# Kernel optimization log

Hardware: AMD Instinct MI355X
Metric: run time of the kernel (lower is better)

## Reference

```python
import jax, jax.numpy as jnp
import numpy as np

L, T, D, H, V, TY, FF = 24, 2048, 512, 16, 1025, 512, 2048
DH = D // H
TOP_K = 15
REP_PEN = 1.35


def _layernorm(x, g, b):
    mu = jnp.mean(x, -1, keepdims=True)
    var = jnp.var(x, -1, keepdims=True)
    return (x - mu) / jnp.sqrt(var + 1e-5) * g + b


def _sine_pe(n, d):
    pos = jnp.arange(n, dtype=jnp.float32)[:, None]
    div = jnp.exp(jnp.arange(0, d, 2, dtype=jnp.float32) * (-np.log(10000.0) / d))
    pe = jnp.zeros((n, d), jnp.float32)
    pe = pe.at[:, 0::2].set(jnp.sin(pos * div))
    pe = pe.at[:, 1::2].set(jnp.cos(pos * div))
    return pe


def setup_inputs() -> dict:
    key = jax.random.key(0)
    ks = jax.random.split(key, 12)
    s = 0.02
    return {
        'y': jax.random.randint(ks[0], (1, TY), 0, V - 1),
        'k_cache': jax.random.normal(ks[1], (L, T, D), jnp.float32),
        'v_cache': jax.random.normal(ks[2], (L, T, D), jnp.float32),
        'y_emb': jax.random.normal(ks[3], (1, TY, D), jnp.float32),
        'tok_emb': jax.random.normal(ks[4], (V, D), jnp.float32) * s,
        'alpha': jnp.ones((1,), jnp.float32),
        'qkv_w': jax.random.normal(ks[5], (L, D, 3 * D), jnp.float32) * s,
        'qkv_b': jnp.zeros((L, 3 * D), jnp.float32),
        'out_w': jax.random.normal(ks[6], (L, D, D), jnp.float32) * s,
        'out_b': jnp.zeros((L, D), jnp.float32),
        'ln1_g': jnp.ones((L, D), jnp.float32),
        'ln1_b': jnp.zeros((L, D), jnp.float32),
        'ff1_w': jax.random.normal(ks[7], (L, D, FF), jnp.float32) * s,
        'ff1_b': jnp.zeros((L, FF), jnp.float32),
        'ff2_w': jax.random.normal(ks[8], (L, FF, D), jnp.float32) * s,
        'ff2_b': jnp.zeros((L, D), jnp.float32),
        'ln2_g': jnp.ones((L, D), jnp.float32),
        'ln2_b': jnp.zeros((L, D), jnp.float32),
        'pred_w': jax.random.normal(ks[9], (D, V), jnp.float32) * s,
    }


def reference(y, k_cache, v_cache, y_emb, tok_emb, alpha, qkv_w, qkv_b, out_w, out_b,
              ln1_g, ln1_b, ff1_w, ff1_b, ff2_w, ff2_b, ln2_g, ln2_b, pred_w):
    # --- embed last generated token, extend y_emb, add learned-alpha sine PE ---
    e = tok_emb[y[0, -1]]                                   # [D]
    y_emb_new = jnp.concatenate([y_emb, e[None, None, :]], axis=1)  # [1, TY+1, D]
    pe = _sine_pe(y_emb_new.shape[1], D)
    y_pos = y_emb_new + alpha[0] * pe[None]
    x = y_pos[0, -1]                                        # [D] single query token

    inv = 1.0 / np.sqrt(DH)

    def step(x, per):
        (qw, qb, ow, ob, g1, b1, w1, bb1, w2, bb2, g2, b2, kl, vl) = per
        qkv = x @ qw + qb
        q, kn, vn = qkv[:D], qkv[D:2 * D], qkv[2 * D:]
        k_all = jnp.concatenate([kl, kn[None]], 0).reshape(-1, H, DH)  # [T+1,H,DH]
        v_all = jnp.concatenate([vl, vn[None]], 0).reshape(-1, H, DH)
        att = jax.nn.softmax(jnp.einsum('hd,thd->ht', q.reshape(H, DH), k_all) * inv, axis=-1)
        o = jnp.einsum('ht,thd->hd', att, v_all).reshape(D)
        x = _layernorm(x + o @ ow + ob, g1, b1)             # post-norm (norm_first=False)
        ff = jax.nn.relu(x @ w1 + bb1) @ w2 + bb2
        x = _layernorm(x + ff, g2, b2)
        return x, (kn, vn)

    xs = (qkv_w, qkv_b, out_w, out_b, ln1_g, ln1_b, ff1_w, ff1_b,
          ff2_w, ff2_b, ln2_g, ln2_b, k_cache, v_cache)
    x, (k_new, v_new) = jax.lax.scan(step, x, xs)

    logits = x @ pred_w                                     # [V]

    # --- sampling pipeline: repetition penalty -> (top_p=1.0 skip) -> top_k -> softmax ---
    prev = y[0]
    score = logits[prev]
    score = jnp.where(score < 0, score * REP_PEN, score / REP_PEN)
    logits = logits.at[prev].set(score)
    vals = jax.lax.top_k(logits, TOP_K)[0]
    logits = jnp.where(logits < vals[-1], -jnp.inf, logits)
    probs = jax.nn.softmax(logits)
    # faithful to torch code: divide probs by standard-normal noise and argmax
    noise = jax.random.normal(jax.random.key(42), (V,), jnp.float32)
    idx_next = jnp.argmax(probs / noise).astype(jnp.int32)
    return probs, idx_next, k_new, v_new
```

## Files before the change

kernel.cpp:

```cpp
#include <hip/hip_runtime.h>
#include <math.h>


#define LNUM 24
#define TPOS 2048
#define DMOD 512
#define HNUM 16
#define VOC  1025
#define TYN  512
#define FFD  2048
#define DHD  32
#define NBLK 256
#define NTHR 256

#define INV_SQRT_DH 0.17677669529663687f


__device__ __forceinline__ unsigned rotl32(unsigned x, int d) {
    return (x << d) | (x >> (32 - d));
}

__device__ float threefry_normal(int i) {
    unsigned c0 = 0u;
    unsigned c1 = (unsigned)i;
    unsigned ks[3];
    ks[0] = 0u; ks[1] = 42u; ks[2] = 0x1BD11BDAu ^ ks[0] ^ ks[1];
    unsigned x0 = c0 + ks[0];
    unsigned x1 = c1 + ks[1];
    const int r0[4] = {13, 15, 26, 6};
    const int r1[4] = {17, 29, 16, 24};
    #pragma unroll
    for (int g = 0; g < 5; ++g) {
        const int* rr = (g & 1) ? r1 : r0;
        #pragma unroll
        for (int j = 0; j < 4; ++j) {
            x0 += x1; x1 = rotl32(x1, rr[j]); x1 ^= x0;
        }
        x0 += ks[(g + 1) % 3];
        x1 += ks[(g + 2) % 3] + (unsigned)(g + 1);
    }
    unsigned bits = x0 ^ x1;
    float u01 = __uint_as_float((bits >> 9) | 0x3f800000u) - 1.0f;
    const float lo = -0.99999994f;
    float u = u01 * (1.0f - lo) + lo;
    u = fmaxf(lo, u);
    float w = -log1pf(-u * u);
    float pp;
    if (w < 5.0f) {
        w = w - 2.5f;
        pp = 2.81022636e-08f;
        pp = fmaf(pp, w, 3.43273939e-07f);
        pp = fmaf(pp, w, -3.5233877e-06f);
        pp = fmaf(pp, w, -4.39150654e-06f);
        pp = fmaf(pp, w, 0.00021858087f);
        pp = fmaf(pp, w, -0.00125372503f);
        pp = fmaf(pp, w, -0.00417768164f);
        pp = fmaf(pp, w, 0.246640727f);
        pp = fmaf(pp, w, 1.50140941f);
    } else {
        w = sqrtf(w) - 3.0f;
        pp = -0.000200214257f;
        pp = fmaf(pp, w, 0.000100950558f);
        pp = fmaf(pp, w, 0.00134934322f);
        pp = fmaf(pp, w, -0.00367342844f);
        pp = fmaf(pp, w, 0.00573950773f);
        pp = fmaf(pp, w, -0.0076224613f);
        pp = fmaf(pp, w, 0.00943887047f);
        pp = fmaf(pp, w, 1.00167406f);
        pp = fmaf(pp, w, 2.83297682f);
    }
    return 1.4142135623730951f * pp * u;
}

__global__ void zero_kernel(float* p, int n) {
    int i = blockIdx.x * blockDim.x + threadIdx.x;
    if (i < n) p[i] = 0.0f;
}

__device__ __forceinline__ float wave_red_sum(float v) {
    #pragma unroll
    for (int o = 32; o; o >>= 1) v += __shfl_xor(v, o, 64);
    return v;
}
__device__ __forceinline__ float wave_red_max(float v) {
    #pragma unroll
    for (int o = 32; o; o >>= 1) v = fmaxf(v, __shfl_xor(v, o, 64));
    return v;
}
__device__ __forceinline__ float block_sum(float v, float* red8, int tid) {
    v = wave_red_sum(v);
    __syncthreads();
    if ((tid & 63) == 0) red8[tid >> 6] = v;
    __syncthreads();
    return red8[0] + red8[1] + red8[2] + red8[3];
}
__device__ __forceinline__ float block_max(float v, float* red8, int tid) {
    v = wave_red_max(v);
    __syncthreads();
    if ((tid & 63) == 0) red8[tid >> 6] = v;
    __syncthreads();
    return fmaxf(fmaxf(red8[0], red8[1]), fmaxf(red8[2], red8[3]));
}

__device__ __forceinline__ float gloadf(const float* p) {
    return __hip_atomic_load((float*)p, __ATOMIC_RELAXED, __HIP_MEMORY_SCOPE_AGENT);
}
__device__ __forceinline__ void gstoref(float* p, float v) {
    __hip_atomic_store(p, v, __ATOMIC_RELAXED, __HIP_MEMORY_SCOPE_AGENT);
}

__device__ __forceinline__ void gsync(unsigned* goB, unsigned* arr,
                                      unsigned& epoch, int tid, int blk) {
    __syncthreads();
    ++epoch;
    if (blk == 0) {
        if (tid > 0) {
            while (__hip_atomic_load(&arr[tid * 16], __ATOMIC_RELAXED,
                                     __HIP_MEMORY_SCOPE_AGENT) < epoch)
                __builtin_amdgcn_s_sleep(1);
        }
        __syncthreads();
        if (tid > 0)
            __hip_atomic_store(&goB[tid * 16], epoch, __ATOMIC_RELAXED,
                               __HIP_MEMORY_SCOPE_AGENT);
    } else {
        if (tid == 0) {
            __hip_atomic_store(&arr[blk * 16], epoch, __ATOMIC_RELAXED,
                               __HIP_MEMORY_SCOPE_AGENT);
            while (__hip_atomic_load(&goB[blk * 16], __ATOMIC_RELAXED,
                                     __HIP_MEMORY_SCOPE_AGENT) < epoch)
                __builtin_amdgcn_s_sleep(1);
        }
        __syncthreads();
    }
}

__device__ __forceinline__ void ln_into(const float* __restrict__ u, const float* __restrict__ g,
                                        const float* __restrict__ b, float* xs, float* red8, int tid) {
    float a = gloadf(u + tid), c = gloadf(u + tid + 256);
    float s1 = block_sum(a + c, red8, tid);
    float s2 = block_sum(a * a + c * c, red8, tid);
    float mu = s1 * (1.0f / DMOD);
    float var = s2 * (1.0f / DMOD) - mu * mu;
    float rstd = rsqrtf(var + 1e-5f);
    xs[tid]       = (a - mu) * rstd * g[tid] + b[tid];
    xs[tid + 256] = (c - mu) * rstd * g[tid + 256] + b[tid + 256];
    __syncthreads();
}

__device__ __forceinline__ void x0_into(const int* __restrict__ y, const float* __restrict__ tokemb,
                                        const float* __restrict__ alpha, float* xs, int tid) {
    int tok = y[TYN - 1];
    #pragma unroll
    for (int r = 0; r < 2; ++r) {
        int d = tid + r * 256;
        float e = tokemb[(size_t)tok * DMOD + d];
        int base = d & ~1;
        float div = expf(-(float)base * (logf(10000.0f) / (float)DMOD));
        float ang = 512.0f * div;
        float pe = (d & 1) ? cosf(ang) : sinf(ang);
        xs[d] = e + alpha[0] * pe;
    }
    __syncthreads();
}


__global__ __launch_bounds__(NTHR) void decode_kernel(
    const int* __restrict__ y, const float* __restrict__ kcache, const float* __restrict__ vcache,
    const float* __restrict__ tokemb, const float* __restrict__ alpha,
    const float* __restrict__ qkvw, const float* __restrict__ qkvbias,
    const float* __restrict__ outw, const float* __restrict__ outb,
    const float* __restrict__ ln1g, const float* __restrict__ ln1b,
    const float* __restrict__ ff1w, const float* __restrict__ ff1b,
    const float* __restrict__ ff2w, const float* __restrict__ ff2b,
    const float* __restrict__ ln2g, const float* __restrict__ ln2b,
    const float* __restrict__ predw, float* __restrict__ out, float* ws)
{
    __shared__ float xs[DMOD];
    __shared__ float red8[8];
    __shared__ float ps[NTHR];
    __shared__ float vred[NTHR];
    __shared__ float qs[DHD];
    __shared__ float os[DHD];
    __shared__ float hs[16];
    __shared__ float redt[NTHR];
    __shared__ float lg[VOC];
    __shared__ float sel[VOC];
    __shared__ unsigned char flagc[VOC];
    __shared__ float rv[4];
    __shared__ int   ri[4];

    int tid = threadIdx.x, blk = blockIdx.x;

    unsigned* goB   = (unsigned*)ws;
    unsigned* arr   = (unsigned*)ws + 4096;
    float* qkv_all  = ws + 8192;
    float* u1_all   = qkv_all + LNUM * 3 * DMOD;
    float* u2_all   = u1_all + LNUM * DMOD;
    float* attnp    = u2_all + LNUM * DMOD;
    float* logits   = attnp + HNUM * 16 * 34;
    unsigned epoch  = 0;

    float* kout = out + 1026;
    float* vout = out + 1026 + (size_t)LNUM * DMOD;

    for (int l = 0; l < LNUM; ++l) {
        const float* u_prev = (l == 0) ? (const float*)0 : (u2_all + (size_t)(l - 1) * DMOD);
        const float* gp = (l == 0) ? (const float*)0 : (ln2g + (size_t)(l - 1) * DMOD);
        const float* bp = (l == 0) ? (const float*)0 : (ln2b + (size_t)(l - 1) * DMOD);
        float* qkvb = qkv_all + (size_t)l * 3 * DMOD;

        if (blk < 192) {
            if (l == 0) x0_into(y, tokemb, alpha, xs, tid);
            else        ln_into(u_prev, gp, bp, xs, red8, tid);
            int cb = blk >> 4, ks = blk & 15;
            int col = cb * 128 + (tid & 127);
            int r0 = ks * 32 + (tid >> 7) * 16;
            const float* wp = qkvw + (size_t)l * DMOD * 3 * DMOD + (size_t)r0 * (3 * DMOD) + col;
            float acc = 0.f;
            #pragma unroll
            for (int i = 0; i < 16; ++i) acc += xs[r0 + i] * wp[(size_t)i * (3 * DMOD)];
            if (ks == 0 && tid < 128) acc += qkvbias[(size_t)l * 3 * DMOD + col];
            atomicAdd(&qkvb[col], acc);
        }
        gsync(goB, arr, epoch, tid, blk);

        {
            int h = blk >> 4, c = blk & 15;
            if (tid < DHD) qs[tid] = gloadf(&qkvb[h * DHD + tid]);
            __syncthreads();
            float sc = -INFINITY;
            if (tid < 128) {
                int pos = c * 128 + tid;
                const float* kp = kcache + (size_t)l * TPOS * DMOD + (size_t)pos * DMOD + h * DHD;
                float s = 0.f;
                #pragma unroll
                for (int d = 0; d < DHD; ++d) s += qs[d] * kp[d];
                sc = s * INV_SQRT_DH;
            } else if (tid == 128 && c == 15) {
                float s = 0.f;
                #pragma unroll
                for (int d = 0; d < DHD; ++d) s += qs[d] * gloadf(&qkvb[DMOD + h * DHD + d]);
                sc = s * INV_SQRT_DH;
            }
            float m = block_max(sc, red8, tid);
            float p = expf(sc - m);
            ps[tid] = p;
            float lsum = block_sum(p, red8, tid);
            int d = tid & (DHD - 1), pg = tid >> 5;
            const float* vbase = vcache + (size_t)l * TPOS * DMOD + (size_t)(c * 128) * DMOD + h * DHD + d;
            float acc = 0.f;
            #pragma unroll
            for (int it = 0; it < 16; ++it) {
                int p2 = pg + it * 8;
                acc += ps[p2] * vbase[(size_t)p2 * DMOD];
            }
            if (c == 15 && pg == 0) acc += ps[128] * gloadf(&qkvb[2 * DMOD + h * DHD + d]);
            vred[tid] = acc;
            __syncthreads();
            float* ap = attnp + (size_t)(h * 16 + c) * 34;
            if (tid < DHD) {
                float a = 0.f;
                #pragma unroll
                for (int g = 0; g < 8; ++g) a += vred[g * DHD + tid];
                gstoref(&ap[2 + tid], a);
            }
            if (tid == 0) { gstoref(&ap[0], m); gstoref(&ap[1], lsum); }
            if (c == 0 && tid < DHD) {
                kout[(size_t)l * DMOD + h * DHD + tid] = gloadf(&qkvb[DMOD + h * DHD + tid]);
                vout[(size_t)l * DMOD + h * DHD + tid] = gloadf(&qkvb[2 * DMOD + h * DHD + tid]);
            }
        }
        gsync(goB, arr, epoch, tid, blk);

        {
            int h = blk >> 4, cg = blk & 15;
            if (h == 0) {
                if (l == 0) x0_into(y, tokemb, alpha, xs, tid);
                else        ln_into(u_prev, gp, bp, xs, red8, tid);
            }
            const float* apb = attnp + (size_t)(h * 16) * 34;
            if (tid < DHD) {
                float M = -INFINITY;
                #pragma unroll
                for (int c = 0; c < 16; ++c) M = fmaxf(M, gloadf(&apb[c * 34]));
                float lsum = 0.f, acc = 0.f;
                #pragma unroll
                for (int c = 0; c < 16; ++c) {
                    float f = expf(gloadf(&apb[c * 34]) - M);
                    lsum += gloadf(&apb[c * 34 + 1]) * f;
                    acc  += gloadf(&apb[c * 34 + 2 + tid]) * f;
                }
                os[tid] = acc / lsum;
            }
            __syncthreads();
            if (tid < 32) {
                int col = cg * 32 + tid;
                const float* wp = outw + (size_t)l * DMOD * DMOD + (size_t)(h * DHD) * DMOD + col;
                float acc2 = 0.f;
                #pragma unroll
                for (int d = 0; d < DHD; ++d) acc2 += os[d] * wp[(size_t)d * DMOD];
                if (h == 0) acc2 += xs[col] + outb[(size_t)l * DMOD + col];
                atomicAdd(&u1_all[(size_t)l * DMOD + col], acc2);
            }
        }
        gsync(goB, arr, epoch, tid, blk);

        if (blk < 128) {
            float* u1l = u1_all + (size_t)l * DMOD;
            float* u2l = u2_all + (size_t)l * DMOD;
            ln_into(u1l, ln1g + (size_t)l * DMOD, ln1b + (size_t)l * DMOD, xs, red8, tid);
            int j0 = blk * 16;
            int jj = tid & 15, dg = tid >> 4;
            const float* wp = ff1w + (size_t)l * DMOD * FFD + (size_t)(dg * 32) * FFD + j0 + jj;
            float acc = 0.f;
            #pragma unroll
            for (int i = 0; i < 32; ++i) acc += xs[dg * 32 + i] * wp[(size_t)i * FFD];
            redt[tid] = acc;
            __syncthreads();
            for (int off = 128; off >= 16; off >>= 1) {
                if (tid < off) redt[tid] += redt[tid + off];
                __syncthreads();
            }
            if (tid < 16) hs[tid] = fmaxf(redt[tid] + ff1b[(size_t)l * FFD + j0 + tid], 0.f);
            __syncthreads();
            const float* w2p = ff2w + (size_t)l * FFD * DMOD + (size_t)j0 * DMOD;
            #pragma unroll
            for (int half = 0; half < 2; ++half) {
                int col = tid + half * 256;
                float a2 = 0.f;
                #pragma unroll
                for (int j = 0; j < 16; ++j) a2 += hs[j] * w2p[(size_t)j * DMOD + col];
                if (blk == 0) a2 += xs[col] + ff2b[(size_t)l * DMOD + col];
                atomicAdd(&u2l[col], a2);
            }
        }
        gsync(goB, arr, epoch, tid, blk);
    }

    {
        const float* u2L = u2_all + (size_t)(LNUM - 1) * DMOD;
        ln_into(u2L, ln2g + (size_t)(LNUM - 1) * DMOD, ln2b + (size_t)(LNUM - 1) * DMOD, xs, red8, tid);
        int c = tid & 3, dg = tid >> 2;
        int col = blk * 4 + c;
        const float* wp = predw + (size_t)(dg * 8) * VOC + col;
        float acc = 0.f;
        #pragma unroll
        for (int i = 0; i < 8; ++i) acc += xs[dg * 8 + i] * wp[(size_t)i * VOC];
        redt[tid] = acc;
        __syncthreads();
        for (int off = 128; off >= 4; off >>= 1) {
            if (tid < off) redt[tid] += redt[tid + off];
            __syncthreads();
        }
        if (tid < 4) gstoref(&logits[blk * 4 + tid], redt[tid]);
        if (blk == 255) {
            __syncthreads();
            float a2 = xs[tid * 2] * predw[(size_t)(tid * 2) * VOC + 1024]
                     + xs[tid * 2 + 1] * predw[(size_t)(tid * 2 + 1) * VOC + 1024];
            redt[tid] = a2;
            __syncthreads();
            for (int off = 128; off >= 1; off >>= 1) {
                if (tid < off) redt[tid] += redt[tid + off];
                __syncthreads();
            }
            if (tid == 0) gstoref(&logits[1024], redt[0]);
        }
    }
    gsync(goB, arr, epoch, tid, blk);

    if (blk != 0) return;

    for (int i = tid; i < VOC; i += NTHR) { lg[i] = gloadf(&logits[i]); flagc[i] = 0; }
    __syncthreads();
    for (int j = tid; j < TYN; j += NTHR) flagc[y[j]] = 1;
    __syncthreads();
    for (int i = tid; i < VOC; i += NTHR) {
        if (flagc[i]) { float v = lg[i]; lg[i] = (v < 0.0f) ? v * 1.35f : v / 1.35f; }
    }
    __syncthreads();
    for (int i = tid; i < VOC; i += NTHR) sel[i] = lg[i];
    __syncthreads();

    float v0 = 0.f, v15 = 0.f;
    for (int k = 0; k < 15; ++k) {
        float bv = -INFINITY; int bi = VOC + 1;
        for (int i = tid; i < VOC; i += NTHR) {
            float v = sel[i];
            if (v > bv) { bv = v; bi = i; }
        }
        #pragma unroll
        for (int o = 32; o; o >>= 1) {
            float v2 = __shfl_xor(bv, o, 64);
            int i2 = __shfl_xor(bi, o, 64);
            if (v2 > bv || (v2 == bv && i2 < bi)) { bv = v2; bi = i2; }
        }
        if ((tid & 63) == 0) { rv[tid >> 6] = bv; ri[tid >> 6] = bi; }
        __syncthreads();
        if (tid == 0) {
            for (int w = 1; w < 4; ++w)
                if (rv[w] > rv[0] || (rv[w] == rv[0] && ri[w] < ri[0])) { rv[0] = rv[w]; ri[0] = ri[w]; }
            sel[ri[0]] = -INFINITY;
        }
        __syncthreads();
        if (k == 0)  v0  = rv[0];
        if (k == 14) v15 = rv[0];
        __syncthreads();
    }

    float se = 0.f;
    for (int i = tid; i < VOC; i += NTHR) {
        float v = lg[i];
        if (!(v < v15)) se += expf(v - v0);
    }
    se = wave_red_sum(se);
    if ((tid & 63) == 0) rv[tid >> 6] = se;
    __syncthreads();
    float total = rv[0] + rv[1] + rv[2] + rv[3];
    __syncthreads();

    float bv = -INFINITY; int bi = VOC + 1;
    for (int i = tid; i < VOC; i += NTHR) {
        float v = lg[i];
        float pr = (v < v15) ? 0.0f : expf(v - v0) / total;
        out[i] = pr;
        float r = pr / threefry_normal(i);
        if (r > bv || (r == bv && i < bi)) { bv = r; bi = i; }
    }
    #pragma unroll
    for (int o = 32; o; o >>= 1) {
        float v2 = __shfl_xor(bv, o, 64);
        int i2 = __shfl_xor(bi, o, 64);
        if (v2 > bv || (v2 == bv && i2 < bi)) { bv = v2; bi = i2; }
    }
    __syncthreads();
    if ((tid & 63) == 0) { rv[tid >> 6] = bv; ri[tid >> 6] = bi; }
    __syncthreads();
    if (tid == 0) {
        for (int w = 1; w < 4; ++w)
            if (rv[w] > rv[0] || (rv[w] == rv[0] && ri[w] < ri[0])) { rv[0] = rv[w]; ri[0] = ri[w]; }
        out[VOC] = (float)ri[0];
    }
}


extern "C" void kernel_launch(void* const* d_in, const int* in_sizes, int n_in,
                              void* d_out, int out_size, void* d_ws, size_t ws_size,
                              hipStream_t stream) {
    const int*   y      = (const int*)d_in[0];
    const float* kcache = (const float*)d_in[1];
    const float* vcache = (const float*)d_in[2];
    const float* tokemb = (const float*)d_in[4];
    const float* alpha  = (const float*)d_in[5];
    const float* qkvw   = (const float*)d_in[6];
    const float* qkvb   = (const float*)d_in[7];
    const float* outw   = (const float*)d_in[8];
    const float* outb   = (const float*)d_in[9];
    const float* ln1g   = (const float*)d_in[10];
    const float* ln1b   = (const float*)d_in[11];
    const float* ff1w   = (const float*)d_in[12];
    const float* ff1b   = (const float*)d_in[13];
    const float* ff2w   = (const float*)d_in[14];
    const float* ff2b   = (const float*)d_in[15];
    const float* ln2g   = (const float*)d_in[16];
    const float* ln2b   = (const float*)d_in[17];
    const float* predw  = (const float*)d_in[18];
    float* outp = (float*)d_out;
    float* wsf  = (float*)d_ws;

    const int ZN = 8192 + LNUM * 3 * DMOD + LNUM * DMOD + LNUM * DMOD;
    zero_kernel<<<(ZN + 255) / 256, 256, 0, stream>>>(wsf, ZN);

    void* args[] = {
        (void*)&y, (void*)&kcache, (void*)&vcache, (void*)&tokemb, (void*)&alpha,
        (void*)&qkvw, (void*)&qkvb, (void*)&outw, (void*)&outb,
        (void*)&ln1g, (void*)&ln1b, (void*)&ff1w, (void*)&ff1b,
        (void*)&ff2w, (void*)&ff2b, (void*)&ln2g, (void*)&ln2b,
        (void*)&predw, (void*)&outp, (void*)&wsf
    };
    hipLaunchCooperativeKernel((const void*)decode_kernel, dim3(NBLK), dim3(NTHR),
                               args, 0, stream);
}
```

Baseline: 968.5 us.

## Prefetch weights and KV tiles into LDS asynchronously ahead of grid barriers

Uses global_load_lds to stream each block's QKV weight slice, K/V cache tile, out-proj slice and FF1/FF2 slices into shared memory one stage before they are needed. The loads are issued before or around the grid barriers, so their latency overlaps synchronisation and the previous stage; next-layer QKV weights are fetched during the FFN stage. Attention scores are recomputed with a wave-shuffle dot product over the LDS K tile. The master-relay grid barrier is replaced by a flat barrier: every block publishes its epoch and all threads poll all flags. The trade-offs are roughly 120KB of LDS per block and heavier polling traffic on the flags.

Result: slower. 1.090 ms (+12.5%).

```diff
diff --git a/kernel.cpp b/kernel.cpp
--- a/kernel.cpp
+++ b/kernel.cpp
@@ -109,30 +109,23 @@
     __hip_atomic_store(p, v, __ATOMIC_RELAXED, __HIP_MEMORY_SCOPE_AGENT);
 }
 
-__device__ __forceinline__ void gsync(unsigned* goB, unsigned* arr,
-                                      unsigned& epoch, int tid, int blk) {
+__device__ __forceinline__ void gl_lds16(const float* g, float* l) {
+    __builtin_amdgcn_global_load_lds(
+        (const __attribute__((address_space(1))) unsigned int*)g,
+        (__attribute__((address_space(3))) unsigned int*)l, 16, 0, 0);
+}
+
+__device__ __forceinline__ void gsync(volatile unsigned* arr, unsigned& epoch,
+                                      int tid, int blk) {
     __syncthreads();
     ++epoch;
-    if (blk == 0) {
-        if (tid > 0) {
-            while (__hip_atomic_load(&arr[tid * 16], __ATOMIC_RELAXED,
-                                     __HIP_MEMORY_SCOPE_AGENT) < epoch)
-                __builtin_amdgcn_s_sleep(1);
-        }
-        __syncthreads();
-        if (tid > 0)
-            __hip_atomic_store(&goB[tid * 16], epoch, __ATOMIC_RELAXED,
-                               __HIP_MEMORY_SCOPE_AGENT);
-    } else {
-        if (tid == 0) {
-            __hip_atomic_store(&arr[blk * 16], epoch, __ATOMIC_RELAXED,
-                               __HIP_MEMORY_SCOPE_AGENT);
-            while (__hip_atomic_load(&goB[blk * 16], __ATOMIC_RELAXED,
-                                     __HIP_MEMORY_SCOPE_AGENT) < epoch)
-                __builtin_amdgcn_s_sleep(1);
-        }
-        __syncthreads();
-    }
+    if (tid == 0)
+        __hip_atomic_store((unsigned*)&arr[blk * 16], epoch, __ATOMIC_RELAXED,
+                           __HIP_MEMORY_SCOPE_AGENT);
+    while (__hip_atomic_load((unsigned*)&arr[tid * 16], __ATOMIC_RELAXED,
+                             __HIP_MEMORY_SCOPE_AGENT) < epoch)
+        __builtin_amdgcn_s_sleep(1);
+    __syncthreads();
 }
 
 __device__ __forceinline__ void ln_into(const float* __restrict__ u, const float* __restrict__ g,
@@ -176,9 +169,14 @@
     const float* __restrict__ ln2g, const float* __restrict__ ln2b,
     const float* __restrict__ predw, float* __restrict__ out, float* ws)
 {
+    __shared__ float qw_lds[4096];
+    __shared__ float kv_lds[8192];
+    __shared__ float ow_lds[1024];
+    __shared__ float f1_lds[8192];
+    __shared__ float f2_lds[8192];
     __shared__ float xs[DMOD];
     __shared__ float red8[8];
-    __shared__ float ps[NTHR];
+    __shared__ float ps[136];
     __shared__ float vred[NTHR];
     __shared__ float qs[DHD];
     __shared__ float os[DHD];
@@ -191,10 +189,10 @@
     __shared__ int   ri[4];
 
     int tid = threadIdx.x, blk = blockIdx.x;
-
-    unsigned* goB   = (unsigned*)ws;
-    unsigned* arr   = (unsigned*)ws + 4096;
-    float* qkv_all  = ws + 8192;
+    int wave = tid >> 6;
+
+    volatile unsigned* arr = (volatile unsigned*)ws;
+    float* qkv_all  = ws + 4096;
     float* u1_all   = qkv_all + LNUM * 3 * DMOD;
     float* u2_all   = u1_all + LNUM * DMOD;
     float* attnp    = u2_all + LNUM * DMOD;
@@ -204,56 +202,101 @@
     float* kout = out + 1026;
     float* vout = out + 1026 + (size_t)LNUM * DMOD;
 
+    if (blk < 192) {
+        int cb = blk >> 4, ks = blk & 15;
+        const float* wb = qkvw + (size_t)(ks * 32) * (3 * DMOD) + cb * 128;
+        #pragma unroll
+        for (int r = 0; r < 4; ++r) {
+            int f = (r * 256 + tid) * 4;
+            int row = f >> 7, col = f & 127;
+            gl_lds16(wb + (size_t)row * (3 * DMOD) + col, qw_lds + (r * 256 + wave * 64) * 4);
+        }
+    }
+    __syncthreads();
+
     for (int l = 0; l < LNUM; ++l) {
         const float* u_prev = (l == 0) ? (const float*)0 : (u2_all + (size_t)(l - 1) * DMOD);
         const float* gp = (l == 0) ? (const float*)0 : (ln2g + (size_t)(l - 1) * DMOD);
         const float* bp = (l == 0) ? (const float*)0 : (ln2b + (size_t)(l - 1) * DMOD);
         float* qkvb = qkv_all + (size_t)l * 3 * DMOD;
-
+        int h = blk >> 4, c = blk & 15;
+
+        {
+            const float* kb = kcache + (size_t)l * TPOS * DMOD + (size_t)(c * 128) * DMOD + h * DHD;
+            const float* vb = vcache + (size_t)l * TPOS * DMOD + (size_t)(c * 128) * DMOD + h * DHD;
+            #pragma unroll
+            for (int r = 0; r < 4; ++r) {
+                int f = (r * 256 + tid) * 4;
+                int row = f >> 5, col = f & 31;
+                gl_lds16(kb + (size_t)row * DMOD + col, kv_lds + (r * 256 + wave * 64) * 4);
+            }
+            #pragma unroll
+            for (int r = 0; r < 4; ++r) {
+                int f = (r * 256 + tid) * 4;
+                int row = f >> 5, col = f & 31;
+                gl_lds16(vb + (size_t)row * DMOD + col, kv_lds + 4096 + (r * 256 + wave * 64) * 4);
+            }
+        }
         if (blk < 192) {
             if (l == 0) x0_into(y, tokemb, alpha, xs, tid);
             else        ln_into(u_prev, gp, bp, xs, red8, tid);
             int cb = blk >> 4, ks = blk & 15;
-            int col = cb * 128 + (tid & 127);
-            int r0 = ks * 32 + (tid >> 7) * 16;
-            const float* wp = qkvw + (size_t)l * DMOD * 3 * DMOD + (size_t)r0 * (3 * DMOD) + col;
+            int cc = tid & 127, rg = tid >> 7;
+            int col = cb * 128 + cc;
             float acc = 0.f;
             #pragma unroll
-            for (int i = 0; i < 16; ++i) acc += xs[r0 + i] * wp[(size_t)i * (3 * DMOD)];
+            for (int i = 0; i < 16; ++i)
+                acc += xs[ks * 32 + rg * 16 + i] * qw_lds[(rg * 16 + i) * 128 + cc];
             if (ks == 0 && tid < 128) acc += qkvbias[(size_t)l * 3 * DMOD + col];
             atomicAdd(&qkvb[col], acc);
         }
-        gsync(goB, arr, epoch, tid, blk);
+        gsync(arr, epoch, tid, blk);
 
         {
-            int h = blk >> 4, c = blk & 15;
+            const float* ob = outw + (size_t)l * DMOD * DMOD + (size_t)(h * DHD) * DMOD + c * 32;
+            {
+                int f = tid * 4;
+                int row = f >> 5, col = f & 31;
+                gl_lds16(ob + (size_t)row * DMOD + col, ow_lds + wave * 64 * 4);
+            }
+            if (blk < 128) {
+                const float* f1 = ff1w + (size_t)l * DMOD * FFD + blk * 16;
+                #pragma unroll
+                for (int r = 0; r < 8; ++r) {
+                    int f = (r * 256 + tid) * 4;
+                    int row = f >> 4, col = f & 15;
+                    gl_lds16(f1 + (size_t)row * FFD + col, f1_lds + (r * 256 + wave * 64) * 4);
+                }
+            }
             if (tid < DHD) qs[tid] = gloadf(&qkvb[h * DHD + tid]);
             __syncthreads();
-            float sc = -INFINITY;
-            if (tid < 128) {
-                int pos = c * 128 + tid;
-                const float* kp = kcache + (size_t)l * TPOS * DMOD + (size_t)pos * DMOD + h * DHD;
-                float s = 0.f;
-                #pragma unroll
-                for (int d = 0; d < DHD; ++d) s += qs[d] * kp[d];
-                sc = s * INV_SQRT_DH;
-            } else if (tid == 128 && c == 15) {
-                float s = 0.f;
-                #pragma unroll
-                for (int d = 0; d < DHD; ++d) s += qs[d] * gloadf(&qkvb[DMOD + h * DHD + d]);
-                sc = s * INV_SQRT_DH;
-            }
-            float m = block_max(sc, red8, tid);
-            float p = expf(sc - m);
-            ps[tid] = p;
-            float lsum = block_sum(p, red8, tid);
-            int d = tid & (DHD - 1), pg = tid >> 5;
-            const float* vbase = vcache + (size_t)l * TPOS * DMOD + (size_t)(c * 128) * DMOD + h * DHD + d;
+            int d = tid & 31, pg = tid >> 5;
+            #pragma unroll
+            for (int it = 0; it < 16; ++it) {
+                int pos = pg + it * 8;
+                float prod = qs[d] * kv_lds[pos * 32 + d];
+                #pragma unroll
+                for (int o = 16; o; o >>= 1) prod += __shfl_xor(prod, o, 64);
+                if (d == 0) ps[pos] = prod * INV_SQRT_DH;
+            }
+            if (c == 15 && tid < 32) {
+                float prod = qs[tid] * gloadf(&qkvb[DMOD + h * DHD + tid]);
+                #pragma unroll
+                for (int o = 16; o; o >>= 1) prod += __shfl_xor(prod, o, 64);
+                if (tid == 0) ps[128] = prod * INV_SQRT_DH;
+            }
+            __syncthreads();
+            int limit = (c == 15) ? 129 : 128;
+            float sv = (tid < limit) ? ps[tid] : -INFINITY;
+            float m = block_max(sv, red8, tid);
+            float pe = expf(sv - m);
+            if (tid < limit) ps[tid] = pe;
+            float lsum = block_sum((tid < limit) ? pe : 0.f, red8, tid);
             float acc = 0.f;
             #pragma unroll
             for (int it = 0; it < 16; ++it) {
                 int p2 = pg + it * 8;
-                acc += ps[p2] * vbase[(size_t)p2 * DMOD];
+                acc += ps[p2] * kv_lds[4096 + p2 * 32 + d];
             }
             if (c == 15 && pg == 0) acc += ps[128] * gloadf(&qkvb[2 * DMOD + h * DHD + d]);
             vred[tid] = acc;
@@ -271,10 +314,17 @@
                 vout[(size_t)l * DMOD + h * DHD + tid] = gloadf(&qkvb[2 * DMOD + h * DHD + tid]);
             }
         }
-        gsync(goB, arr, epoch, tid, blk);
+        gsync(arr, epoch, tid, blk);
 
         {
-            int h = blk >> 4, cg = blk & 15;
+            if (blk < 128) {
+                const float* f2 = ff2w + (size_t)l * FFD * DMOD + (size_t)(blk * 16) * DMOD;
+                #pragma unroll
+                for (int r = 0; r < 8; ++r) {
+                    int f = (r * 256 + tid) * 4;
+                    gl_lds16(f2 + f, f2_lds + (r * 256 + wave * 64) * 4);
+                }
+            }
             if (h == 0) {
                 if (l == 0) x0_into(y, tokemb, alpha, xs, tid);
                 else        ln_into(u_prev, gp, bp, xs, red8, tid);
@@ -283,66 +333,76 @@
             if (tid < DHD) {
                 float M = -INFINITY;
                 #pragma unroll
-                for (int c = 0; c < 16; ++c) M = fmaxf(M, gloadf(&apb[c * 34]));
+                for (int cc = 0; cc < 16; ++cc) M = fmaxf(M, gloadf(&apb[cc * 34]));
                 float lsum = 0.f, acc = 0.f;
                 #pragma unroll
-                for (int c = 0; c < 16; ++c) {
-                    float f = expf(gloadf(&apb[c * 34]) - M);
-                    lsum += gloadf(&apb[c * 34 + 1]) * f;
-                    acc  += gloadf(&apb[c * 34 + 2 + tid]) * f;
+                for (int cc = 0; cc < 16; ++cc) {
+                    float f = expf(gloadf(&apb[cc * 34]) - M);
+                    lsum += gloadf(&apb[cc * 34 + 1]) * f;
+                    acc  += gloadf(&apb[cc * 34 + 2 + tid]) * f;
                 }
                 os[tid] = acc / lsum;
             }
             __syncthreads();
             if (tid < 32) {
-                int col = cg * 32 + tid;
-                const float* wp = outw + (size_t)l * DMOD * DMOD + (size_t)(h * DHD) * DMOD + col;
+                int col = c * 32 + tid;
                 float acc2 = 0.f;
                 #pragma unroll
-                for (int d = 0; d < DHD; ++d) acc2 += os[d] * wp[(size_t)d * DMOD];
+                for (int d = 0; d < DHD; ++d) acc2 += os[d] * ow_lds[d * 32 + tid];
                 if (h == 0) acc2 += xs[col] + outb[(size_t)l * DMOD + col];
                 atomicAdd(&u1_all[(size_t)l * DMOD + col], acc2);
             }
         }
-        gsync(goB, arr, epoch, tid, blk);
-
-        if (blk < 128) {
-            float* u1l = u1_all + (size_t)l * DMOD;
-            float* u2l = u2_all + (size_t)l * DMOD;
-            ln_into(u1l, ln1g + (size_t)l * DMOD, ln1b + (size_t)l * DMOD, xs, red8, tid);
-            int j0 = blk * 16;
-            int jj = tid & 15, dg = tid >> 4;
-            const float* wp = ff1w + (size_t)l * DMOD * FFD + (size_t)(dg * 32) * FFD + j0 + jj;
-            float acc = 0.f;
-            #pragma unroll
-            for (int i = 0; i < 32; ++i) acc += xs[dg * 32 + i] * wp[(size_t)i * FFD];
-            redt[tid] = acc;
-            __syncthreads();
-            for (int off = 128; off >= 16; off >>= 1) {
-                if (tid < off) redt[tid] += redt[tid + off];
+        gsync(arr, epoch, tid, blk);
+
+        {
+            if (l + 1 < LNUM && blk < 192) {
+                int cb = blk >> 4, ks = blk & 15;
+                const float* wb = qkvw + (size_t)(l + 1) * DMOD * 3 * DMOD
+                                + (size_t)(ks * 32) * (3 * DMOD) + cb * 128;
+                #pragma unroll
+                for (int r = 0; r < 4; ++r) {
+                    int f = (r * 256 + tid) * 4;
+                    int row = f >> 7, col = f & 127;
+                    gl_lds16(wb + (size_t)row * (3 * DMOD) + col, qw_lds + (r * 256 + wave * 64) * 4);
+                }
+            }
+            if (blk < 128) {
+                float* u1l = u1_all + (size_t)l * DMOD;
+                float* u2l = u2_all + (size_t)l * DMOD;
+                ln_into(u1l, ln1g + (size_t)l * DMOD, ln1b + (size_t)l * DMOD, xs, red8, tid);
+                int jj = tid & 15, dg = tid >> 4;
+                float acc = 0.f;
+                #pragma unroll
+                for (int i = 0; i < 32; ++i)
+                    acc += xs[dg * 32 + i] * f1_lds[(dg * 32 + i) * 16 + jj];
+                redt[tid] = acc;
                 __syncthreads();
-            }
-            if (tid < 16) hs[tid] = fmaxf(redt[tid] + ff1b[(size_t)l * FFD + j0 + tid], 0.f);
-            __syncthreads();
-            const float* w2p = ff2w + (size_t)l * FFD * DMOD + (size_t)j0 * DMOD;
-            #pragma unroll
-            for (int half = 0; half < 2; ++half) {
-                int col = tid + half * 256;
-                float a2 = 0.f;
-                #pragma unroll
-                for (int j = 0; j < 16; ++j) a2 += hs[j] * w2p[(size_t)j * DMOD + col];
-                if (blk == 0) a2 += xs[col] + ff2b[(size_t)l * DMOD + col];
-                atomicAdd(&u2l[col], a2);
-            }
-        }
-        gsync(goB, arr, epoch, tid, blk);
+                for (int off = 128; off >= 16; off >>= 1) {
+                    if (tid < off) redt[tid] += redt[tid + off];
+                    __syncthreads();
+                }
+                if (tid < 16) hs[tid] = fmaxf(redt[tid] + ff1b[(size_t)l * FFD + blk * 16 + tid], 0.f);
+                __syncthreads();
+                #pragma unroll
+                for (int half = 0; half < 2; ++half) {
+                    int col = tid + half * 256;
+                    float a2 = 0.f;
+                    #pragma unroll
+                    for (int j = 0; j < 16; ++j) a2 += hs[j] * f2_lds[j * 512 + col];
+                    if (blk == 0) a2 += xs[col] + ff2b[(size_t)l * DMOD + col];
+                    atomicAdd(&u2l[col], a2);
+                }
+            }
+        }
+        gsync(arr, epoch, tid, blk);
     }
 
     {
         const float* u2L = u2_all + (size_t)(LNUM - 1) * DMOD;
         ln_into(u2L, ln2g + (size_t)(LNUM - 1) * DMOD, ln2b + (size_t)(LNUM - 1) * DMOD, xs, red8, tid);
-        int c = tid & 3, dg = tid >> 2;
-        int col = blk * 4 + c;
+        int cc = tid & 3, dg = tid >> 2;
+        int col = blk * 4 + cc;
         const float* wp = predw + (size_t)(dg * 8) * VOC + col;
         float acc = 0.f;
         #pragma unroll
@@ -367,7 +427,7 @@
             if (tid == 0) gstoref(&logits[1024], redt[0]);
         }
     }
-    gsync(goB, arr, epoch, tid, blk);
+    gsync(arr, epoch, tid, blk);
 
     if (blk != 0) return;
 
@@ -468,7 +528,7 @@
     float* outp = (float*)d_out;
     float* wsf  = (float*)d_ws;
 
-    const int ZN = 8192 + LNUM * 3 * DMOD + LNUM * DMOD + LNUM * DMOD;
+    const int ZN = 4096 + LNUM * 3 * DMOD + LNUM * DMOD + LNUM * DMOD;
     zero_kernel<<<(ZN + 255) / 256, 256, 0, stream>>>(wsf, ZN);
 
     void* args[] = {
```
